# Performance work log

Hardware: AMD Instinct MI355X
Metric: run time of the kernel (lower is better)

## Reference

```python
import jax, jax.numpy as jnp
import numpy as np
import math

B, S, F, R = 16, 2048, 512, 4
EPS = 1e-5

def setup_inputs() -> dict:
    key = jax.random.key(0)
    ks = jax.random.split(key, 8)
    s = 1.0 / math.sqrt(S)
    return {
        "x": jax.random.normal(ks[0], (B, S, F), dtype=jnp.float32),
        "Wq": jax.random.uniform(ks[1], (R, S), jnp.float32, -s, s),
        "bq": jnp.zeros((R,), jnp.float32),
        "Wk": jax.random.uniform(ks[2], (R, S), jnp.float32, -s, s),
        "bk": jnp.zeros((R,), jnp.float32),
        "Wv": jax.random.uniform(ks[3], (S, S), jnp.float32, -s, s),
        "bv": jnp.zeros((S,), jnp.float32),
        "ln_w": jnp.ones((S, F), jnp.float32),
        "ln_b": jnp.zeros((S, F), jnp.float32),
        "alpha": jnp.asarray(0.1, jnp.float32),
        "beta": jnp.asarray(0.1, jnp.float32),
    }

def reference(x, Wq, bq, Wk, bk, Wv, bv, ln_w, ln_b, alpha, beta):
    # LayerNorm over last two dims [S, F]
    mu = jnp.mean(x, axis=(1, 2), keepdims=True)
    var = jnp.mean(jnp.square(x - mu), axis=(1, 2), keepdims=True)
    x_norm = (x - mu) * jax.lax.rsqrt(var + EPS) * ln_w + ln_b
    x_t = jnp.swapaxes(x_norm, 1, 2)  # [B, F, S]
    Q = jnp.einsum('bfs,rs->bfr', x_t, Wq) + bq  # [B, F, R]
    K = jnp.einsum('bfs,rs->bfr', x_t, Wk) + bk  # [B, F, R]
    A = jnp.einsum('bfr,bgr->bfg', Q, K) / math.sqrt(R)  # [B, F, F]
    A = jax.nn.softmax(A, axis=-1)
    V = jnp.einsum('bfs,ts->bft', x_t, Wv) + bv  # [B, F, S]
    out = jnp.einsum('bfg,bgs->bfs', A, V)  # [B, F, S]
    # dropout in eval mode = identity
    out = x_t + alpha * out + V + beta * V
    return jnp.swapaxes(out, 1, 2)  # [B, S, F]
```

## Files before the change

kernel.cpp:

```cpp
#include <hip/hip_runtime.h>
#include <hip/hip_bf16.h>

#define NB 16
#define SS 2048
#define FF 512

typedef __bf16 bf16_t;
typedef __bf16 bf16x8 __attribute__((ext_vector_type(8)));
typedef __bf16 bf16x4 __attribute__((ext_vector_type(4)));
typedef float  f32x4  __attribute__((ext_vector_type(4)));

__global__ __launch_bounds__(256) void stats_kernel(const float* __restrict__ x,
                                                    float* __restrict__ partials) {
    const int b = blockIdx.y;
    const float* xb = x + ((size_t)b << 20) + (size_t)blockIdx.x * 16384;
    float s = 0.0f, ss = 0.0f;
#pragma unroll
    for (int i = 0; i < 16; ++i) {
        const float4 v = *(const float4*)&xb[(threadIdx.x + i * 256) * 4];
        s  += v.x + v.y + v.z + v.w;
        ss += v.x * v.x + v.y * v.y + v.z * v.z + v.w * v.w;
    }
#pragma unroll
    for (int off = 32; off > 0; off >>= 1) {
        s  += __shfl_down(s, off);
        ss += __shfl_down(ss, off);
    }
    __shared__ float ps[4], pss[4];
    const int w = threadIdx.x >> 6, lane = threadIdx.x & 63;
    if (lane == 0) { ps[w] = s; pss[w] = ss; }
    __syncthreads();
    if (threadIdx.x == 0) {
        partials[b * 64 + blockIdx.x]        = ps[0] + ps[1] + ps[2] + ps[3];
        partials[1024 + b * 64 + blockIdx.x] = pss[0] + pss[1] + pss[2] + pss[3];
    }
}

__global__ __launch_bounds__(256) void finalize_stats(const float* __restrict__ partials,
                                                      float* __restrict__ musig) {
    const int tid = threadIdx.x;
    const int b = tid >> 4, i = tid & 15;
    float s = 0.f, ss = 0.f;
#pragma unroll
    for (int j = 0; j < 4; ++j) {
        s  += partials[b * 64 + i * 4 + j];
        ss += partials[1024 + b * 64 + i * 4 + j];
    }
#pragma unroll
    for (int off = 8; off > 0; off >>= 1) {
        s  += __shfl_xor(s, off);
        ss += __shfl_xor(ss, off);
    }
    if (i == 0) {
        const float inv_n = 1.0f / 1048576.0f;
        const float mu  = s * inv_n;
        const float var = ss * inv_n - mu * mu;
        musig[b]      = mu;
        musig[16 + b] = rsqrtf(var + 1e-5f);
    }
}

__global__ __launch_bounds__(256) void ynorm_kernel(const float* __restrict__ x,
                                                    const float* __restrict__ lw,
                                                    const float* __restrict__ lb,
                                                    const float* __restrict__ musig,
                                                    bf16_t* __restrict__ Y) {
    __shared__ bf16_t t[32][33];
    const int b = blockIdx.z;
    const int f0 = blockIdx.x * 32, s0 = blockIdx.y * 32;
    const float mu = musig[b], rs = musig[16 + b];
    const int c = threadIdx.x & 31, rb = threadIdx.x >> 5;
#pragma unroll
    for (int i = 0; i < 4; ++i) {
        const int s_loc = rb + i * 8;
        const size_t idx = (size_t)(s0 + s_loc) * FF + f0 + c;
        const float yv = (x[((size_t)b << 20) + idx] - mu) * rs * lw[idx] + lb[idx];
        t[s_loc][c] = (bf16_t)yv;
    }
    __syncthreads();
#pragma unroll
    for (int i = 0; i < 4; ++i) {
        const int f_loc = rb + i * 8;
        Y[((size_t)b << 20) + (size_t)(f0 + f_loc) * SS + s0 + c] = t[c][f_loc];
    }
}

__global__ __launch_bounds__(256) void cast_wv(const float* __restrict__ Wv,
                                               bf16_t* __restrict__ Wvb) {
    const size_t i = ((size_t)blockIdx.x * 256 + threadIdx.x) * 4;
    const float4 v = *(const float4*)&Wv[i];
    bf16x4 o;
    o[0] = (bf16_t)v.x; o[1] = (bf16_t)v.y; o[2] = (bf16_t)v.z; o[3] = (bf16_t)v.w;
    *(bf16x4*)&Wvb[i] = o;
}

__global__ __launch_bounds__(256) void qk_kernel(const bf16_t* __restrict__ Y,
                                                 const float* __restrict__ Wq,
                                                 const float* __restrict__ bq,
                                                 const float* __restrict__ Wk,
                                                 const float* __restrict__ bk,
                                                 float* __restrict__ Qo,
                                                 float* __restrict__ Ko) {
    const int w = threadIdx.x >> 6, lane = threadIdx.x & 63;
    const int row = blockIdx.x * 4 + w;
    const bf16_t* y = Y + (size_t)row * SS;
    float qa[4] = {0.f, 0.f, 0.f, 0.f}, ka[4] = {0.f, 0.f, 0.f, 0.f};
#pragma unroll
    for (int c = 0; c < 4; ++c) {
        const int s = c * 512 + lane * 8;
        const bf16x8 yv = *(const bf16x8*)&y[s];
        float yf[8];
#pragma unroll
        for (int j = 0; j < 8; ++j) yf[j] = (float)yv[j];
#pragma unroll
        for (int r = 0; r < 4; ++r) {
            const float4 a0 = *(const float4*)&Wq[r * SS + s];
            const float4 a1 = *(const float4*)&Wq[r * SS + s + 4];
            const float4 c0 = *(const float4*)&Wk[r * SS + s];
            const float4 c1 = *(const float4*)&Wk[r * SS + s + 4];
            qa[r] += yf[0]*a0.x + yf[1]*a0.y + yf[2]*a0.z + yf[3]*a0.w
                   + yf[4]*a1.x + yf[5]*a1.y + yf[6]*a1.z + yf[7]*a1.w;
            ka[r] += yf[0]*c0.x + yf[1]*c0.y + yf[2]*c0.z + yf[3]*c0.w
                   + yf[4]*c1.x + yf[5]*c1.y + yf[6]*c1.z + yf[7]*c1.w;
        }
    }
#pragma unroll
    for (int off = 32; off > 0; off >>= 1) {
#pragma unroll
        for (int r = 0; r < 4; ++r) {
            qa[r] += __shfl_down(qa[r], off);
            ka[r] += __shfl_down(ka[r], off);
        }
    }
    if (lane == 0) {
#pragma unroll
        for (int r = 0; r < 4; ++r) {
            Qo[(size_t)row * 4 + r] = qa[r] + bq[r];
            Ko[(size_t)row * 4 + r] = ka[r] + bk[r];
        }
    }
}

__global__ __launch_bounds__(256) void softmax_kernel(const float* __restrict__ Qo,
                                                      const float* __restrict__ Ko,
                                                      bf16_t* __restrict__ Aout) {
    const int w = threadIdx.x >> 6, lane = threadIdx.x & 63;
    const int row = blockIdx.x * 4 + w;
    const int b = row >> 9;
    const float4 q = *(const float4*)&Qo[(size_t)row * 4];
    const float* kb = Ko + (size_t)b * FF * 4;
    float sc[8];
#pragma unroll
    for (int j = 0; j < 8; ++j) {
        const float4 kv = *(const float4*)&kb[(lane * 8 + j) * 4];
        sc[j] = (q.x*kv.x + q.y*kv.y + q.z*kv.z + q.w*kv.w) * 0.5f;
    }
    float mx = sc[0];
#pragma unroll
    for (int j = 1; j < 8; ++j) mx = fmaxf(mx, sc[j]);
#pragma unroll
    for (int off = 32; off > 0; off >>= 1) mx = fmaxf(mx, __shfl_xor(mx, off));
    float sum = 0.f;
#pragma unroll
    for (int j = 0; j < 8; ++j) { sc[j] = __expf(sc[j] - mx); sum += sc[j]; }
#pragma unroll
    for (int off = 32; off > 0; off >>= 1) sum += __shfl_xor(sum, off);
    const float inv = 1.0f / sum;
    bf16x8 o;
#pragma unroll
    for (int j = 0; j < 8; ++j) o[j] = (bf16_t)(sc[j] * inv);
    *(bf16x8*)&Aout[(size_t)row * FF + lane * 8] = o;
}

__global__ __launch_bounds__(512, 2) void gemm_nt_8phase(
        const bf16_t* __restrict__ Abase, long long strideA, int lda,
        const bf16_t* __restrict__ Bbase, long long strideB, int ldb,
        bf16_t* __restrict__ Cbase, long long strideC, int ldc,
        int NTILES, const float* __restrict__ bias_m) {
    __shared__ __align__(16) bf16_t As[2][16384];
    __shared__ __align__(16) bf16_t Bs[2][16384];
    const int tid = threadIdx.x;
    const int w = tid >> 6, lane = tid & 63;

    const int nchunk = gridDim.x >> 3;
    const int wgid = (blockIdx.x & 7) * nchunk + (blockIdx.x >> 3);
    const int bz = wgid >> 4;
    const int rem = wgid & 15;
    const int m0 = (rem & 7) * 256, n0 = (rem >> 3) * 256;

    const bf16_t* A = Abase + (size_t)bz * (size_t)strideA;
    const bf16_t* B = Bbase + (size_t)bz * (size_t)strideB;
    bf16_t* C = Cbase + (size_t)bz * (size_t)strideC;
    const int wm = w >> 2, wn = w & 3;

    const int rr0 = (w * 2 + 0) * 16 + (lane >> 2);
    const int rr1 = (w * 2 + 1) * 16 + (lane >> 2);
    const int sw0 = ((lane & 3) ^ ((rr0 >> 1) & 3)) * 8;
    const int sw1 = ((lane & 3) ^ ((rr1 >> 1) & 3)) * 8;
    const bf16_t* gA0 = A + (size_t)(m0 + rr0) * lda + sw0;
    const bf16_t* gA1 = A + (size_t)(m0 + rr1) * lda + sw1;
    const bf16_t* gB0 = B + (size_t)(n0 + rr0) * ldb + sw0;
    const bf16_t* gB1 = B + (size_t)(n0 + rr1) * ldb + sw1;
    const int d0 = (w * 2 + 0) * 512;
    const int d1 = (w * 2 + 1) * 512;

#define STA(bi, h, ko) do {                                                          \
    __builtin_amdgcn_global_load_lds(                                                \
        (const __attribute__((address_space(1))) unsigned int*)(gA0 + (ko) + (h)*32),\
        (__attribute__((address_space(3))) unsigned int*)&As[bi][(h)*8192 + d0], 16, 0, 0); \
    __builtin_amdgcn_global_load_lds(                                                \
        (const __attribute__((address_space(1))) unsigned int*)(gA1 + (ko) + (h)*32),\
        (__attribute__((address_space(3))) unsigned int*)&As[bi][(h)*8192 + d1], 16, 0, 0); \
} while (0)
#define STB(bi, h, ko) do {                                                          \
    __builtin_amdgcn_global_load_lds(                                                \
        (const __attribute__((address_space(1))) unsigned int*)(gB0 + (ko) + (h)*32),\
        (__attribute__((address_space(3))) unsigned int*)&Bs[bi][(h)*8192 + d0], 16, 0, 0); \
    __builtin_amdgcn_global_load_lds(                                                \
        (const __attribute__((address_space(1))) unsigned int*)(gB1 + (ko) + (h)*32),\
        (__attribute__((address_space(3))) unsigned int*)&Bs[bi][(h)*8192 + d1], 16, 0, 0); \
} while (0)

    const int cs = lane >> 4;
    int offA[2][8], offB[2][4];
#pragma unroll
    for (int kk = 0; kk < 2; ++kk) {
#pragma unroll
        for (int mt = 0; mt < 8; ++mt) {
            const int r = wm * 128 + mt * 16 + (lane & 15);
            offA[kk][mt] = kk * 8192 + r * 32 + ((cs ^ ((r >> 1) & 3)) << 3);
        }
#pragma unroll
        for (int nt = 0; nt < 4; ++nt) {
            const int r = wn * 64 + nt * 16 + (lane & 15);
            offB[kk][nt] = kk * 8192 + r * 32 + ((cs ^ ((r >> 1) & 3)) << 3);
        }
    }

#define DS_A(kk, mh) do { _Pragma("unroll")                                   \
    for (int i = 0; i < 4; ++i) af[i] = *(const bf16x8*)&as[offA[kk][(mh)*4 + i]]; } while (0)
#define DS_B(kk) do { _Pragma("unroll")                                       \
    for (int i = 0; i < 4; ++i) bfr[i] = *(const bf16x8*)&bs[offB[kk][i]]; } while (0)
#define MFMA16(mh) do { _Pragma("unroll")                                     \
    for (int i = 0; i < 4; ++i) { _Pragma("unroll")                           \
        for (int nt = 0; nt < 4; ++nt)                                        \
            acc[(mh)*4 + i][nt] = __builtin_amdgcn_mfma_f32_16x16x32_bf16(    \
                af[i], bfr[nt], acc[(mh)*4 + i][nt], 0, 0, 0); } } while (0)
#define VM4   asm volatile("s_waitcnt vmcnt(4)" ::: "memory")
#define HBAR  __builtin_amdgcn_s_barrier()
#define LGKM0 do { asm volatile("s_waitcnt lgkmcnt(0)" ::: "memory");         \
                   __builtin_amdgcn_sched_barrier(0); } while (0)
#define SBAR  __builtin_amdgcn_sched_barrier(0)
#define PRIO1 __builtin_amdgcn_s_setprio(1)
#define PRIO0 __builtin_amdgcn_s_setprio(0)

    f32x4 acc[8][4] = {};
    const int mask = NTILES - 1;

    STA(0, 0, 0); STB(0, 0, 0); STA(0, 1, 0); STB(0, 1, 0);
    VM4; HBAR;

    for (int t = 0; t < NTILES; ++t) {
        const int oth = (t & 1) ^ 1;
        const int ko = ((t + 1) & mask) * 64;
        const bf16_t* as = As[t & 1];
        const bf16_t* bs = Bs[t & 1];
        bf16x8 af[4], bfr[4];
        DS_A(0, 0); DS_B(0); SBAR;
        STA(oth, 0, ko); SBAR;
        HBAR;
        LGKM0;
        PRIO1; MFMA16(0); PRIO0; SBAR;
        HBAR;
        DS_A(0, 1); SBAR;
        STB(oth, 0, ko); SBAR;
        VM4;
        HBAR;
        LGKM0;
        PRIO1; MFMA16(1); PRIO0; SBAR;
        HBAR;
        DS_A(1, 0); DS_B(1); SBAR;
        STA(oth, 1, ko); SBAR;
        HBAR;
        LGKM0;
        PRIO1; MFMA16(0); PRIO0; SBAR;
        HBAR;
        DS_A(1, 1); SBAR;
        STB(oth, 1, ko); SBAR;
        VM4;
        HBAR;
        LGKM0;
        PRIO1; MFMA16(1); PRIO0; SBAR;
        HBAR;
    }
#undef STA
#undef STB
#undef DS_A
#undef DS_B
#undef MFMA16
#undef VM4
#undef HBAR
#undef LGKM0
#undef SBAR
#undef PRIO1
#undef PRIO0

#pragma unroll
    for (int mt = 0; mt < 8; ++mt) {
#pragma unroll
        for (int r = 0; r < 4; ++r) {
            const int row = m0 + wm * 128 + mt * 16 + ((lane >> 4) << 2) + r;
            const float bm = bias_m ? bias_m[row] : 0.0f;
#pragma unroll
            for (int nt = 0; nt < 4; ++nt) {
                const int col = n0 + wn * 64 + nt * 16 + (lane & 15);
                C[(size_t)row * ldc + col] = (bf16_t)(acc[mt][nt][r] + bm);
            }
        }
    }
}

__global__ __launch_bounds__(256) void epilogue_kernel(const float* __restrict__ x,
                                                       const float* __restrict__ lw,
                                                       const float* __restrict__ lb,
                                                       const bf16_t* __restrict__ Ot,
                                                       const bf16_t* __restrict__ Vt,
                                                       const float* __restrict__ musig,
                                                       const float* __restrict__ alphap,
                                                       const float* __restrict__ betap,
                                                       float* __restrict__ out) {
    const size_t i4 = ((size_t)blockIdx.x * 256 + threadIdx.x) * 4;
    const size_t b = i4 >> 20;
    const size_t rr = i4 & 1048575;
    const float mu = musig[b], rs = musig[16 + b];
    const float alpha = alphap[0];
    const float onepb = 1.0f + betap[0];
    const float4 xv  = *(const float4*)&x[i4];
    const float4 wv  = *(const float4*)&lw[rr];
    const float4 bbv = *(const float4*)&lb[rr];
    const bf16x4 ov = *(const bf16x4*)&Ot[i4];
    const bf16x4 vv = *(const bf16x4*)&Vt[i4];
    float4 o;
    o.x = (xv.x - mu) * rs * wv.x + bbv.x + alpha * (float)ov[0] + onepb * (float)vv[0];
    o.y = (xv.y - mu) * rs * wv.y + bbv.y + alpha * (float)ov[1] + onepb * (float)vv[1];
    o.z = (xv.z - mu) * rs * wv.z + bbv.z + alpha * (float)ov[2] + onepb * (float)vv[2];
    o.w = (xv.w - mu) * rs * wv.w + bbv.w + alpha * (float)ov[3] + onepb * (float)vv[3];
    *(float4*)&out[i4] = o;
}

extern "C" void kernel_launch(void* const* d_in, const int* in_sizes, int n_in,
                              void* d_out, int out_size, void* d_ws, size_t ws_size,
                              hipStream_t stream) {
    const float* x   = (const float*)d_in[0];
    const float* Wq  = (const float*)d_in[1];
    const float* bq  = (const float*)d_in[2];
    const float* Wk  = (const float*)d_in[3];
    const float* bk  = (const float*)d_in[4];
    const float* Wv  = (const float*)d_in[5];
    const float* bv  = (const float*)d_in[6];
    const float* lw  = (const float*)d_in[7];
    const float* lb  = (const float*)d_in[8];
    const float* alp = (const float*)d_in[9];
    const float* bet = (const float*)d_in[10];
    float* out = (float*)d_out;

    char* ws = (char*)d_ws;
    float*  musig = (float*)(ws + 128);
    float*  Qo    = (float*)(ws + 256);
    float*  Ko    = (float*)(ws + 256 + 131072);
    bf16_t* Wvb   = (bf16_t*)(ws + 262400);
    bf16_t* Asm   = (bf16_t*)(ws + 8651008);
    float*  partials = (float*)(ws + 8651008);
    bf16_t* Vt    = (bf16_t*)(ws + 17039616);
    bf16_t* Y     = (bf16_t*)(ws + 50594048);
    bf16_t* Ot    = Y;

    stats_kernel<<<dim3(64, 16), 256, 0, stream>>>(x, partials);
    finalize_stats<<<1, 256, 0, stream>>>(partials, musig);
    cast_wv<<<4096, 256, 0, stream>>>(Wv, Wvb);
    ynorm_kernel<<<dim3(16, 64, 16), 256, 0, stream>>>(x, lw, lb, musig, Y);
    qk_kernel<<<2048, 256, 0, stream>>>(Y, Wq, bq, Wk, bk, Qo, Ko);
    softmax_kernel<<<2048, 256, 0, stream>>>(Qo, Ko, Asm);
    gemm_nt_8phase<<<256, 512, 0, stream>>>(
        Wvb, 0, SS, Y, 1 << 20, SS, Vt, 1 << 20, FF, 32, bv);
    gemm_nt_8phase<<<256, 512, 0, stream>>>(
        Vt, 1 << 20, FF, Asm, FF * FF, FF, Ot, 1 << 20, FF, 8, nullptr);
    epilogue_kernel<<<16384, 256, 0, stream>>>(x, lw, lb, Ot, Vt, musig, alp, bet, out);
}
```

Measured before the change: 195.1 us.

## Fuse residual epilogue into second GEMM and simplify main-loop pipeline

The separate elementwise epilogue kernel is folded into the A·V GEMM as a templated epilogue that reads x, ln weights, and V, then writes the final fp32 output directly. This removes the bf16 Ot round-trip and one kernel launch. The hand-tuned 8-phase interleaved loop with setprio, partial vmcnt waits and fine-grained barriers is replaced by a simpler loop. That loop issues all next-tile global loads up front, does the MFMAs, then waits with vmcnt(0) plus a barrier, which may reduce overlap. The fused epilogue does scalar, strided fp32 loads and stores in the MFMA accumulator layout, so it is less coalesced than the old float4 kernel.

```diff
diff --git a/kernel.cpp b/kernel.cpp
--- a/kernel.cpp
+++ b/kernel.cpp
@@ -172,11 +172,16 @@
     *(bf16x8*)&Aout[(size_t)row * FF + lane * 8] = o;
 }
 
-__global__ __launch_bounds__(512, 2) void gemm_nt_8phase(
+template<bool FUSE>
+__global__ __launch_bounds__(512, 2) void gemm_nt_tile(
         const bf16_t* __restrict__ Abase, long long strideA, int lda,
         const bf16_t* __restrict__ Bbase, long long strideB, int ldb,
         bf16_t* __restrict__ Cbase, long long strideC, int ldc,
-        int NTILES, const float* __restrict__ bias_m) {
+        int NTILES, const float* __restrict__ bias_m,
+        const float* __restrict__ xp, const float* __restrict__ lwp,
+        const float* __restrict__ lbp, const float* __restrict__ musig,
+        const float* __restrict__ alphap, const float* __restrict__ betap,
+        float* __restrict__ outp) {
     __shared__ __align__(16) bf16_t As[2][16384];
     __shared__ __align__(16) bf16_t Bs[2][16384];
     const int tid = threadIdx.x;
@@ -237,115 +242,78 @@
         }
     }
 
-#define DS_A(kk, mh) do { _Pragma("unroll")                                   \
-    for (int i = 0; i < 4; ++i) af[i] = *(const bf16x8*)&as[offA[kk][(mh)*4 + i]]; } while (0)
-#define DS_B(kk) do { _Pragma("unroll")                                       \
-    for (int i = 0; i < 4; ++i) bfr[i] = *(const bf16x8*)&bs[offB[kk][i]]; } while (0)
-#define MFMA16(mh) do { _Pragma("unroll")                                     \
-    for (int i = 0; i < 4; ++i) { _Pragma("unroll")                           \
-        for (int nt = 0; nt < 4; ++nt)                                        \
-            acc[(mh)*4 + i][nt] = __builtin_amdgcn_mfma_f32_16x16x32_bf16(    \
-                af[i], bfr[nt], acc[(mh)*4 + i][nt], 0, 0, 0); } } while (0)
-#define VM4   asm volatile("s_waitcnt vmcnt(4)" ::: "memory")
-#define HBAR  __builtin_amdgcn_s_barrier()
-#define LGKM0 do { asm volatile("s_waitcnt lgkmcnt(0)" ::: "memory");         \
-                   __builtin_amdgcn_sched_barrier(0); } while (0)
-#define SBAR  __builtin_amdgcn_sched_barrier(0)
-#define PRIO1 __builtin_amdgcn_s_setprio(1)
-#define PRIO0 __builtin_amdgcn_s_setprio(0)
-
     f32x4 acc[8][4] = {};
     const int mask = NTILES - 1;
 
     STA(0, 0, 0); STB(0, 0, 0); STA(0, 1, 0); STB(0, 1, 0);
-    VM4; HBAR;
+    asm volatile("s_waitcnt vmcnt(0)\n\ts_barrier" ::: "memory");
 
     for (int t = 0; t < NTILES; ++t) {
         const int oth = (t & 1) ^ 1;
         const int ko = ((t + 1) & mask) * 64;
+        STA(oth, 0, ko); STB(oth, 0, ko); STA(oth, 1, ko); STB(oth, 1, ko);
+        __builtin_amdgcn_sched_barrier(0);
         const bf16_t* as = As[t & 1];
         const bf16_t* bs = Bs[t & 1];
-        bf16x8 af[4], bfr[4];
-        DS_A(0, 0); DS_B(0); SBAR;
-        STA(oth, 0, ko); SBAR;
-        HBAR;
-        LGKM0;
-        PRIO1; MFMA16(0); PRIO0; SBAR;
-        HBAR;
-        DS_A(0, 1); SBAR;
-        STB(oth, 0, ko); SBAR;
-        VM4;
-        HBAR;
-        LGKM0;
-        PRIO1; MFMA16(1); PRIO0; SBAR;
-        HBAR;
-        DS_A(1, 0); DS_B(1); SBAR;
-        STA(oth, 1, ko); SBAR;
-        HBAR;
-        LGKM0;
-        PRIO1; MFMA16(0); PRIO0; SBAR;
-        HBAR;
-        DS_A(1, 1); SBAR;
-        STB(oth, 1, ko); SBAR;
-        VM4;
-        HBAR;
-        LGKM0;
-        PRIO1; MFMA16(1); PRIO0; SBAR;
-        HBAR;
+#pragma unroll
+        for (int kk = 0; kk < 2; ++kk) {
+            bf16x8 bfr[4];
+#pragma unroll
+            for (int i = 0; i < 4; ++i) bfr[i] = *(const bf16x8*)&bs[offB[kk][i]];
+#pragma unroll
+            for (int mh = 0; mh < 2; ++mh) {
+                bf16x8 af[4];
+#pragma unroll
+                for (int i = 0; i < 4; ++i) af[i] = *(const bf16x8*)&as[offA[kk][mh * 4 + i]];
+#pragma unroll
+                for (int i = 0; i < 4; ++i)
+#pragma unroll
+                    for (int nt = 0; nt < 4; ++nt)
+                        acc[mh * 4 + i][nt] = __builtin_amdgcn_mfma_f32_16x16x32_bf16(
+                            af[i], bfr[nt], acc[mh * 4 + i][nt], 0, 0, 0);
+            }
+        }
+        asm volatile("s_waitcnt vmcnt(0)\n\ts_barrier" ::: "memory");
     }
 #undef STA
 #undef STB
-#undef DS_A
-#undef DS_B
-#undef MFMA16
-#undef VM4
-#undef HBAR
-#undef LGKM0
-#undef SBAR
-#undef PRIO1
-#undef PRIO0
-
-#pragma unroll
-    for (int mt = 0; mt < 8; ++mt) {
-#pragma unroll
-        for (int r = 0; r < 4; ++r) {
-            const int row = m0 + wm * 128 + mt * 16 + ((lane >> 4) << 2) + r;
-            const float bm = bias_m ? bias_m[row] : 0.0f;
-#pragma unroll
-            for (int nt = 0; nt < 4; ++nt) {
-                const int col = n0 + wn * 64 + nt * 16 + (lane & 15);
-                C[(size_t)row * ldc + col] = (bf16_t)(acc[mt][nt][r] + bm);
+
+    if constexpr (!FUSE) {
+#pragma unroll
+        for (int mt = 0; mt < 8; ++mt) {
+#pragma unroll
+            for (int r = 0; r < 4; ++r) {
+                const int row = m0 + wm * 128 + mt * 16 + ((lane >> 4) << 2) + r;
+                const float bm = bias_m ? bias_m[row] : 0.0f;
+#pragma unroll
+                for (int nt = 0; nt < 4; ++nt) {
+                    const int col = n0 + wn * 64 + nt * 16 + (lane & 15);
+                    C[(size_t)row * ldc + col] = (bf16_t)(acc[mt][nt][r] + bm);
+                }
             }
         }
-    }
-}
-
-__global__ __launch_bounds__(256) void epilogue_kernel(const float* __restrict__ x,
-                                                       const float* __restrict__ lw,
-                                                       const float* __restrict__ lb,
-                                                       const bf16_t* __restrict__ Ot,
-                                                       const bf16_t* __restrict__ Vt,
-                                                       const float* __restrict__ musig,
-                                                       const float* __restrict__ alphap,
-                                                       const float* __restrict__ betap,
-                                                       float* __restrict__ out) {
-    const size_t i4 = ((size_t)blockIdx.x * 256 + threadIdx.x) * 4;
-    const size_t b = i4 >> 20;
-    const size_t rr = i4 & 1048575;
-    const float mu = musig[b], rs = musig[16 + b];
-    const float alpha = alphap[0];
-    const float onepb = 1.0f + betap[0];
-    const float4 xv  = *(const float4*)&x[i4];
-    const float4 wv  = *(const float4*)&lw[rr];
-    const float4 bbv = *(const float4*)&lb[rr];
-    const bf16x4 ov = *(const bf16x4*)&Ot[i4];
-    const bf16x4 vv = *(const bf16x4*)&Vt[i4];
-    float4 o;
-    o.x = (xv.x - mu) * rs * wv.x + bbv.x + alpha * (float)ov[0] + onepb * (float)vv[0];
-    o.y = (xv.y - mu) * rs * wv.y + bbv.y + alpha * (float)ov[1] + onepb * (float)vv[1];
-    o.z = (xv.z - mu) * rs * wv.z + bbv.z + alpha * (float)ov[2] + onepb * (float)vv[2];
-    o.w = (xv.w - mu) * rs * wv.w + bbv.w + alpha * (float)ov[3] + onepb * (float)vv[3];
-    *(float4*)&out[i4] = o;
+    } else {
+        const float mu = musig[bz], rs = musig[16 + bz];
+        const float alpha = alphap[0];
+        const float onepb = 1.0f + betap[0];
+        const float* xb = xp + ((size_t)bz << 20);
+        float* ob = outp + ((size_t)bz << 20);
+#pragma unroll
+        for (int mt = 0; mt < 8; ++mt) {
+#pragma unroll
+            for (int r = 0; r < 4; ++r) {
+                const int row = m0 + wm * 128 + mt * 16 + ((lane >> 4) << 2) + r;
+#pragma unroll
+                for (int nt = 0; nt < 4; ++nt) {
+                    const int col = n0 + wn * 64 + nt * 16 + (lane & 15);
+                    const size_t idx = (size_t)row * FF + col;
+                    const float xn = (xb[idx] - mu) * rs * lwp[idx] + lbp[idx];
+                    const float v = (float)A[(size_t)row * lda + col];
+                    ob[idx] = xn + alpha * acc[mt][nt][r] + onepb * v;
+                }
+            }
+        }
+    }
 }
 
 extern "C" void kernel_launch(void* const* d_in, const int* in_sizes, int n_in,
@@ -373,7 +341,6 @@
     float*  partials = (float*)(ws + 8651008);
     bf16_t* Vt    = (bf16_t*)(ws + 17039616);
     bf16_t* Y     = (bf16_t*)(ws + 50594048);
-    bf16_t* Ot    = Y;
 
     stats_kernel<<<dim3(64, 16), 256, 0, stream>>>(x, partials);
     finalize_stats<<<1, 256, 0, stream>>>(partials, musig);
@@ -381,9 +348,10 @@
     ynorm_kernel<<<dim3(16, 64, 16), 256, 0, stream>>>(x, lw, lb, musig, Y);
     qk_kernel<<<2048, 256, 0, stream>>>(Y, Wq, bq, Wk, bk, Qo, Ko);
     softmax_kernel<<<2048, 256, 0, stream>>>(Qo, Ko, Asm);
-    gemm_nt_8phase<<<256, 512, 0, stream>>>(
-        Wvb, 0, SS, Y, 1 << 20, SS, Vt, 1 << 20, FF, 32, bv);
-    gemm_nt_8phase<<<256, 512, 0, stream>>>(
-        Vt, 1 << 20, FF, Asm, FF * FF, FF, Ot, 1 << 20, FF, 8, nullptr);
-    epilogue_kernel<<<16384, 256, 0, stream>>>(x, lw, lb, Ot, Vt, musig, alp, bet, out);
-}
+    gemm_nt_tile<false><<<256, 512, 0, stream>>>(
+        Wvb, 0, SS, Y, 1 << 20, SS, Vt, 1 << 20, FF, 32, bv,
+        nullptr, nullptr, nullptr, nullptr, nullptr, nullptr, nullptr);
+    gemm_nt_tile<true><<<256, 512, 0, stream>>>(
+        Vt, 1 << 20, FF, Asm, FF * FF, FF, nullptr, 0, FF, 8, nullptr,
+        x, lw, lb, musig, alp, bet, out);
+}
```

New measurement: 205.1 us. 5.1% more time.
